# Performance work log

Hardware: AMD Instinct MI355X
Metric: run time of the kernel (lower is better)

## Reference

```python
import jax, jax.numpy as jnp
import numpy as np

B, T, C, H = 4, 2048, 1024, 16
D = C // H


def setup_inputs() -> dict:
    key = jax.random.key(0)
    ks = jax.random.split(key, 6)
    s = 1.0 / np.sqrt(C)
    return {
        "x": jax.random.normal(ks[0], (B, T, C), dtype=jnp.float32),
        "attention_mask": jnp.ones((B, 1, T), dtype=jnp.int32),
        "Wq": jax.random.normal(ks[1], (C, C), dtype=jnp.float32) * s,
        "bq": jnp.zeros((C,), dtype=jnp.float32),
        "Wk": jax.random.normal(ks[2], (C, C), dtype=jnp.float32) * s,
        "bk": jnp.zeros((C,), dtype=jnp.float32),
        "Wv": jax.random.normal(ks[3], (C, C), dtype=jnp.float32) * s,
        "bv": jnp.zeros((C,), dtype=jnp.float32),
        "Wp": jax.random.normal(ks[4], (C, C), dtype=jnp.float32) * s,
        "bp": jnp.zeros((C,), dtype=jnp.float32),
    }


def reference(x, attention_mask, Wq, bq, Wk, bk, Wv, bv, Wp, bp):
    b, t, c = x.shape
    d = c // H
    # projections (torch Linear: x @ W^T + b)
    q = (x @ Wq.T + bq).reshape(b, t, H, d).transpose(0, 2, 1, 3)  # [B,H,T,D]
    k = (x @ Wk.T + bk).reshape(b, t, H, d).transpose(0, 2, 1, 3)
    v = (x @ Wv.T + bv).reshape(b, t, H, d).transpose(0, 2, 1, 3)
    attn = jnp.einsum("bhqd,bhkd->bhqk", q, k) / jnp.sqrt(jnp.asarray(d, x.dtype))
    mask = attention_mask[:, :, :t]  # [B,1,T] -> broadcast over [B,H,T,T] keys
    attn = jnp.where(mask[:, :, None, :] == 0, jnp.asarray(-jnp.inf, x.dtype), attn)
    attn = jax.nn.softmax(attn, axis=-1)  # dropout p=0 (eval)
    y = jnp.einsum("bhqk,bhkd->bhqd", attn, v)
    y = y.transpose(0, 2, 1, 3).reshape(b, t, c)
    return y @ Wp.T + bp
```

## Files before the change

### kernel.cpp

```cpp
#include <hip/hip_runtime.h>


#define TT 2048
#define CC 1024
#define HH 16
#define DD 64
#define BB 4

typedef unsigned short u16;
typedef unsigned int u32;
typedef __attribute__((ext_vector_type(8))) short bf16x8;
typedef __attribute__((ext_vector_type(4))) float f32x4;

#if __has_builtin(__builtin_amdgcn_exp2f)
#define EXP2(x) __builtin_amdgcn_exp2f(x)
#else
#define EXP2(x) __expf((x) * 0.6931471805599453f)
#endif

__device__ __forceinline__ u16 f2bf(float f) {
    u32 u = __builtin_bit_cast(u32, f);
    u += 0x7FFFu + ((u >> 16) & 1u);
    return (u16)(u >> 16);
}
__device__ __forceinline__ u32 pk2(float a, float b) {
    u32 ua = __builtin_bit_cast(u32, a); ua += 0x7FFFu + ((ua >> 16) & 1u);
    u32 ub = __builtin_bit_cast(u32, b); ub += 0x7FFFu + ((ub >> 16) & 1u);
    return __builtin_amdgcn_perm(ub, ua, 0x07060302);
}

#define GLDS(g, l) __builtin_amdgcn_global_load_lds( \
    (const __attribute__((address_space(1))) void*)(g), \
    (__attribute__((address_space(3))) void*)(l), 16, 0, 0)

__global__ __launch_bounds__(256) void wcvt(const float* __restrict__ s,
                                            u16* __restrict__ d, int n8) {
    const int i = blockIdx.x * 256 + threadIdx.x;
    if (i < n8) {
        const float4 f0 = ((const float4*)s)[2 * i];
        const float4 f1 = ((const float4*)s)[2 * i + 1];
        uint4 w;
        w.x = pk2(f0.x, f0.y); w.y = pk2(f0.z, f0.w);
        w.z = pk2(f1.x, f1.y); w.w = pk2(f1.z, f1.w);
        ((uint4*)d)[i] = w;
    }
}

__global__ __launch_bounds__(256) void wcvt3(const float* __restrict__ s0,
                                             const float* __restrict__ s1,
                                             const float* __restrict__ s2,
                                             u16* __restrict__ d0,
                                             u16* __restrict__ d1,
                                             u16* __restrict__ d2, int n8) {
    const int which = blockIdx.y;
    const float* s = (which == 0) ? s0 : (which == 1) ? s1 : s2;
    u16* d = (which == 0) ? d0 : (which == 1) ? d1 : d2;
    const int i = blockIdx.x * 256 + threadIdx.x;
    if (i < n8) {
        const float4 f0 = ((const float4*)s)[2 * i];
        const float4 f1 = ((const float4*)s)[2 * i + 1];
        uint4 w;
        w.x = pk2(f0.x, f0.y); w.y = pk2(f0.z, f0.w);
        w.z = pk2(f1.x, f1.y); w.w = pk2(f1.z, f1.w);
        ((uint4*)d)[i] = w;
    }
}

template <int PROJ>
__global__ __launch_bounds__(256) void gemmX(const u16* __restrict__ A,
                                             const u16* __restrict__ Wb,
                                             const float* __restrict__ b0,
                                             const float* __restrict__ b1,
                                             const float* __restrict__ b2,
                                             void* __restrict__ out0,
                                             void* __restrict__ out1,
                                             void* __restrict__ out2) {
    __shared__ u16 As[128 * 64];
    __shared__ u16 Bs[128 * 64];

    const int tid  = threadIdx.x;
    const int wave = tid >> 6, lane = tid & 63;
    const int quad = lane >> 4, l16 = lane & 15;
    const int bm = blockIdx.y * 128, bn = blockIdx.x * 128;
    const int wm = (wave >> 1) * 64, wn = (wave & 1) * 64;
    const int K = CC;

    f32x4 acc[4][4] = {};

    for (int k0 = 0; k0 < K; k0 += 64) {
#pragma unroll
        for (int rr = 0; rr < 4; rr++) {
            const int c = rr * 256 + tid;
            const int row = c >> 3;
            const int cs = ((c & 7) ^ (row & 7)) * 8;
            GLDS(&Wb[(size_t)(bn + row) * K + k0 + cs], &Bs[c * 8]);
        }
#pragma unroll
        for (int rr = 0; rr < 4; rr++) {
            const int c = rr * 256 + tid;
            const int row = c >> 3;
            const int cs = ((c & 7) ^ (row & 7)) * 8;
            GLDS(&A[(size_t)(bm + row) * K + k0 + cs], &As[c * 8]);
        }
        __syncthreads();

#pragma unroll
        for (int ks = 0; ks < 2; ks++) {
            bf16x8 af[4], bfr[4];
#pragma unroll
            for (int i = 0; i < 4; i++) {
                const int row = wm + i * 16 + l16;
                const int s8 = (ks * 4 + quad) ^ (row & 7);
                af[i] = *(bf16x8*)&As[row * 64 + s8 * 8];
            }
#pragma unroll
            for (int j = 0; j < 4; j++) {
                const int row = wn + j * 16 + l16;
                const int s8 = (ks * 4 + quad) ^ (row & 7);
                bfr[j] = *(bf16x8*)&Bs[row * 64 + s8 * 8];
            }
#pragma unroll
            for (int i = 0; i < 4; i++)
#pragma unroll
                for (int j = 0; j < 4; j++)
                    acc[i][j] = __builtin_amdgcn_mfma_f32_16x16x32_bf16(af[i], bfr[j], acc[i][j], 0, 0, 0);
        }
        __syncthreads();
    }

    if (PROJ) {
        float* out = (float*)out0;
#pragma unroll
        for (int j = 0; j < 4; j++) {
            const int col = bn + wn + j * 16 + l16;
            const float bv = b0[col];
#pragma unroll
            for (int i = 0; i < 4; i++) {
                const int row0 = bm + wm + i * 16 + quad * 4;
#pragma unroll
                for (int r = 0; r < 4; r++)
                    out[(size_t)(row0 + r) * CC + col] = acc[i][j][r] + bv;
            }
        }
    } else {
        const int mid = bn >> 10;
        const float* bias = (mid == 0) ? b0 : (mid == 1) ? b1 : b2;
#pragma unroll
        for (int j = 0; j < 4; j++) {
            const int col  = bn + wn + j * 16 + l16;
            const int colL = col & (CC - 1);
            const float bv = bias[colL];
#pragma unroll
            for (int i = 0; i < 4; i++) {
                const int row0 = bm + wm + i * 16 + quad * 4;
                if (mid < 2) {
                    u16* out = (u16*)(mid ? out1 : out0);
#pragma unroll
                    for (int r = 0; r < 4; r++)
                        out[(size_t)(row0 + r) * CC + colL] = f2bf(acc[i][j][r] + bv);
                } else {
                    const int hh = colL >> 6, dch = colL & 63;
                    const int bb = row0 >> 11, t0 = row0 & (TT - 1);
                    const size_t idx = (((size_t)bb * HH + hh) * DD + dch) * TT + t0;
                    uint2 w;
                    w.x = pk2(acc[i][j][0] + bv, acc[i][j][1] + bv);
                    w.y = pk2(acc[i][j][2] + bv, acc[i][j][3] + bv);
                    *(uint2*)&((u16*)out2)[idx] = w;
                }
            }
        }
    }
}

__global__ __launch_bounds__(256) void attn(const u16* __restrict__ Q,
                                            const u16* __restrict__ Kb,
                                            const u16* __restrict__ Vt,
                                            const int* __restrict__ mask,
                                            u16* __restrict__ Y) {
    const int b = blockIdx.z, h = blockIdx.y, qt = blockIdx.x;
    const int tid  = threadIdx.x;
    const int wave = tid >> 6, lane = tid & 63;
    const int quad = lane >> 4, l16 = lane & 15;
    const int qrow0 = qt * 128 + wave * 32;

    __shared__ u16 Ks[2][64 * 64];
    __shared__ u16 Vs[2][64 * 64];
    __shared__ u16 Plds[4][32][72];

    const size_t qb = ((size_t)b * TT + qrow0) * CC + h * DD;

    bf16x8 qf[2][2];
#pragma unroll
    for (int m = 0; m < 2; m++)
#pragma unroll
        for (int ks = 0; ks < 2; ks++)
            qf[m][ks] = *(const bf16x8*)&Q[qb + (size_t)(m * 16 + l16) * CC + ks * 32 + quad * 8];

    const int c0 = tid, c1 = tid + 256;
    const int r0 = c0 >> 3, r1 = c1 >> 3;
    const int kp0 = (c0 & 7) ^ ((r0 >> 2) & 7), kp1 = (c1 & 7) ^ ((r1 >> 2) & 7);
    const int vp0 = (c0 & 7) ^ (r0 & 7),        vp1 = (c1 & 7) ^ (r1 & 7);
    const u16* kgp = Kb + ((size_t)b * TT) * CC + h * DD;
    const u16* vgp = Vt + ((size_t)(b * HH + h) * DD) * TT;
    const int* mp = mask + b * TT + 4 * l16;

    f32x4 o[2][4] = {};
    float lsum[2][4] = {};
    const float SC = 0.18033688011112042f;

    GLDS(&kgp[(size_t)r0 * CC + kp0 * 8], &Ks[0][c0 * 8]);
    GLDS(&kgp[(size_t)r1 * CC + kp1 * 8], &Ks[0][c1 * 8]);
    GLDS(&vgp[(size_t)r0 * TT + vp0 * 8], &Vs[0][c0 * 8]);
    GLDS(&vgp[(size_t)r1 * TT + vp1 * 8], &Vs[0][c1 * 8]);
    asm volatile("s_waitcnt vmcnt(0)" ::: "memory");
    __builtin_amdgcn_s_barrier();
    __builtin_amdgcn_sched_barrier(0);

#pragma unroll 1
    for (int kt = 0; kt < TT; kt += 64) {
        const int cur = (kt >> 6) & 1;
        const u16* Kc = &Ks[cur][0];
        const u16* Vc = &Vs[cur][0];

        const int4 mv = *(const int4*)&mp[kt];

        if (kt + 64 < TT) {
            const int nxt = cur ^ 1;
            GLDS(&kgp[(size_t)(kt + 64 + r0) * CC + kp0 * 8], &Ks[nxt][c0 * 8]);
            GLDS(&kgp[(size_t)(kt + 64 + r1) * CC + kp1 * 8], &Ks[nxt][c1 * 8]);
            GLDS(&vgp[(size_t)r0 * TT + kt + 64 + vp0 * 8], &Vs[nxt][c0 * 8]);
            GLDS(&vgp[(size_t)r1 * TT + kt + 64 + vp1 * 8], &Vs[nxt][c1 * 8]);
        }

        f32x4 s[2][4] = {};
        __builtin_amdgcn_s_setprio(1);
#pragma unroll
        for (int n = 0; n < 4; n++) {
#pragma unroll
            for (int ks = 0; ks < 2; ks++) {
                const int krow = 4 * l16 + n;
                const int pos = (ks * 4 + quad) ^ ((krow >> 2) & 7);
                const bf16x8 kf = *(bf16x8*)&Kc[krow * 64 + pos * 8];
#pragma unroll
                for (int m = 0; m < 2; m++)
                    s[m][n] = __builtin_amdgcn_mfma_f32_16x16x32_bf16(qf[m][ks], kf, s[m][n], 0, 0, 0);
            }
        }
        __builtin_amdgcn_s_setprio(0);

        float bb[4];
        bb[0] = mv.x ? 0.f : -1e38f;
        bb[1] = mv.y ? 0.f : -1e38f;
        bb[2] = mv.z ? 0.f : -1e38f;
        bb[3] = mv.w ? 0.f : -1e38f;

#pragma unroll
        for (int m = 0; m < 2; m++)
#pragma unroll
            for (int r = 0; r < 4; r++) {
                const float p0 = EXP2(fmaf(s[m][0][r], SC, bb[0]));
                const float p1 = EXP2(fmaf(s[m][1][r], SC, bb[1]));
                const float p2 = EXP2(fmaf(s[m][2][r], SC, bb[2]));
                const float p3 = EXP2(fmaf(s[m][3][r], SC, bb[3]));
                lsum[m][r] += (p0 + p1) + (p2 + p3);
                uint2 w; w.x = pk2(p0, p1); w.y = pk2(p2, p3);
                *(uint2*)&Plds[wave][m * 16 + quad * 4 + r][4 * l16] = w;
            }

        __builtin_amdgcn_s_setprio(1);
#pragma unroll
        for (int ks = 0; ks < 2; ks++) {
            bf16x8 pf[2];
#pragma unroll
            for (int m = 0; m < 2; m++)
                pf[m] = *(bf16x8*)&Plds[wave][m * 16 + l16][ks * 32 + quad * 8];
#pragma unroll
            for (int dt = 0; dt < 4; dt++) {
                const int vrow = dt * 16 + l16;
                const int pos = (ks * 4 + quad) ^ (vrow & 7);
                const bf16x8 vf = *(bf16x8*)&Vc[vrow * 64 + pos * 8];
#pragma unroll
                for (int m = 0; m < 2; m++)
                    o[m][dt] = __builtin_amdgcn_mfma_f32_16x16x32_bf16(pf[m], vf, o[m][dt], 0, 0, 0);
            }
        }
        __builtin_amdgcn_s_setprio(0);

        asm volatile("s_waitcnt vmcnt(0)" ::: "memory");
        __builtin_amdgcn_sched_barrier(0);
        __builtin_amdgcn_s_barrier();
    }

#pragma unroll
    for (int off = 1; off < 16; off <<= 1)
#pragma unroll
        for (int m = 0; m < 2; m++)
#pragma unroll
            for (int r = 0; r < 4; r++) lsum[m][r] += __shfl_xor(lsum[m][r], off, 64);

#pragma unroll
    for (int m = 0; m < 2; m++) {
        float inv[4];
#pragma unroll
        for (int r = 0; r < 4; r++) inv[r] = 1.0f / lsum[m][r];
#pragma unroll
        for (int dt = 0; dt < 4; dt++)
#pragma unroll
            for (int r = 0; r < 4; r++)
                Y[qb + (size_t)(m * 16 + quad * 4 + r) * CC + dt * 16 + l16] = f2bf(o[m][dt][r] * inv[r]);
    }
}

extern "C" void kernel_launch(void* const* d_in, const int* in_sizes, int n_in,
                              void* d_out, int out_size, void* d_ws, size_t ws_size,
                              hipStream_t stream) {
    const float* x    = (const float*)d_in[0];
    const int*   mask = (const int*)d_in[1];
    const float* Wq   = (const float*)d_in[2];
    const float* bq   = (const float*)d_in[3];
    const float* Wk   = (const float*)d_in[4];
    const float* bk   = (const float*)d_in[5];
    const float* Wv   = (const float*)d_in[6];
    const float* bv   = (const float*)d_in[7];
    const float* Wp   = (const float*)d_in[8];
    const float* bp   = (const float*)d_in[9];

    u16* ws = (u16*)d_ws;
    const size_t sz = (size_t)BB * TT * CC;
    u16* Qb   = ws;
    u16* Kbuf = ws + sz;
    u16* Vtb  = ws + 2 * sz;

    u16* xb   = (u16*)d_out;
    u16* Wq16 = xb + sz;
    u16* Wk16 = Wq16 + (size_t)CC * CC;
    u16* Wv16 = Wk16 + (size_t)CC * CC;

    const int W8 = CC * CC / 8;
    wcvt<<<4096, 256, 0, stream>>>(x, xb, (int)(sz / 8));
    wcvt3<<<dim3(512, 3), 256, 0, stream>>>(Wq, Wk, Wv, Wq16, Wk16, Wv16, W8);

    gemmX<0><<<dim3(24, 64), 256, 0, stream>>>(xb, Wq16, bq, bk, bv, Qb, Kbuf, Vtb);

    attn<<<dim3(TT / 128, HH, BB), 256, 0, stream>>>(Qb, Kbuf, Vtb, mask, Qb);

    wcvt<<<512, 256, 0, stream>>>(Wp, Kbuf, W8);
    gemmX<1><<<dim3(8, 64), 256, 0, stream>>>(Qb, Kbuf, bp, nullptr, nullptr, d_out, nullptr, nullptr);
}
```

Baseline: 310.3 us.

## Compute transposed QK^T scores to keep P in registers, skipping LDS round trip

```diff
diff --git a/kernel.cpp b/kernel.cpp
--- a/kernel.cpp
+++ b/kernel.cpp
@@ -11,6 +11,7 @@
 typedef unsigned int u32;
 typedef __attribute__((ext_vector_type(8))) short bf16x8;
 typedef __attribute__((ext_vector_type(4))) float f32x4;
+typedef __attribute__((ext_vector_type(4))) u32 u32x4;
 
 #if __has_builtin(__builtin_amdgcn_exp2f)
 #define EXP2(x) __builtin_amdgcn_exp2f(x)
@@ -27,6 +28,11 @@
     u32 ua = __builtin_bit_cast(u32, a); ua += 0x7FFFu + ((ua >> 16) & 1u);
     u32 ub = __builtin_bit_cast(u32, b); ub += 0x7FFFu + ((ub >> 16) & 1u);
     return __builtin_amdgcn_perm(ub, ua, 0x07060302);
+}
+__device__ __forceinline__ u32 cvtpk(float lo, float hi) {
+    u32 r;
+    asm("v_cvt_pk_bf16_f32 %0, %1, %2" : "=v"(r) : "v"(lo), "v"(hi));
+    return r;
 }
 
 #define GLDS(g, l) __builtin_amdgcn_global_load_lds( \
@@ -185,7 +191,7 @@
 
     __shared__ u16 Ks[2][64 * 64];
     __shared__ u16 Vs[2][64 * 64];
-    __shared__ u16 Plds[4][32][72];
+    __shared__ __align__(16) float bias_lds[TT];
 
     const size_t qb = ((size_t)b * TT + qrow0) * CC + h * DD;
 
@@ -196,23 +202,40 @@
         for (int ks = 0; ks < 2; ks++)
             qf[m][ks] = *(const bf16x8*)&Q[qb + (size_t)(m * 16 + l16) * CC + ks * 32 + quad * 8];
 
+    {
+        const int i = tid * 8;
+        const int4 m0 = *(const int4*)&mask[b * TT + i];
+        const int4 m1 = *(const int4*)&mask[b * TT + i + 4];
+        bias_lds[i + 0] = m0.x ? 0.f : -1e38f;
+        bias_lds[i + 1] = m0.y ? 0.f : -1e38f;
+        bias_lds[i + 2] = m0.z ? 0.f : -1e38f;
+        bias_lds[i + 3] = m0.w ? 0.f : -1e38f;
+        bias_lds[i + 4] = m1.x ? 0.f : -1e38f;
+        bias_lds[i + 5] = m1.y ? 0.f : -1e38f;
+        bias_lds[i + 6] = m1.z ? 0.f : -1e38f;
+        bias_lds[i + 7] = m1.w ? 0.f : -1e38f;
+    }
+
     const int c0 = tid, c1 = tid + 256;
     const int r0 = c0 >> 3, r1 = c1 >> 3;
-    const int kp0 = (c0 & 7) ^ ((r0 >> 2) & 7), kp1 = (c1 & 7) ^ ((r1 >> 2) & 7);
-    const int vp0 = (c0 & 7) ^ (r0 & 7),        vp1 = (c1 & 7) ^ (r1 & 7);
+    const int kp0 = (c0 & 7) ^ ((((r0 >> 3) & 1) << 2) | (r0 & 3));
+    const int kp1 = (c1 & 7) ^ ((((r1 >> 3) & 1) << 2) | (r1 & 3));
+    const int vp0 = (c0 & 7) ^ (r0 & 7), vp1 = (c1 & 7) ^ (r1 & 7);
     const u16* kgp = Kb + ((size_t)b * TT) * CC + h * DD;
     const u16* vgp = Vt + ((size_t)(b * HH + h) * DD) * TT;
-    const int* mp = mask + b * TT + 4 * l16;
+
+    const int rowA = ((l16 >> 2) << 3) | (l16 & 3);
+    const int s0k  = (((l16 >> 2) & 1) << 2) | (l16 & 3);
 
     f32x4 o[2][4] = {};
-    float lsum[2][4] = {};
+    float lsum[2] = {};
     const float SC = 0.18033688011112042f;
 
     GLDS(&kgp[(size_t)r0 * CC + kp0 * 8], &Ks[0][c0 * 8]);
     GLDS(&kgp[(size_t)r1 * CC + kp1 * 8], &Ks[0][c1 * 8]);
     GLDS(&vgp[(size_t)r0 * TT + vp0 * 8], &Vs[0][c0 * 8]);
     GLDS(&vgp[(size_t)r1 * TT + vp1 * 8], &Vs[0][c1 * 8]);
-    asm volatile("s_waitcnt vmcnt(0)" ::: "memory");
+    asm volatile("s_waitcnt vmcnt(0) lgkmcnt(0)" ::: "memory");
     __builtin_amdgcn_s_barrier();
     __builtin_amdgcn_sched_barrier(0);
 
@@ -221,8 +244,6 @@
         const int cur = (kt >> 6) & 1;
         const u16* Kc = &Ks[cur][0];
         const u16* Vc = &Vs[cur][0];
-
-        const int4 mv = *(const int4*)&mp[kt];
 
         if (kt + 64 < TT) {
             const int nxt = cur ^ 1;
@@ -232,53 +253,60 @@
             GLDS(&vgp[(size_t)r1 * TT + kt + 64 + vp1 * 8], &Vs[nxt][c1 * 8]);
         }
 
-        f32x4 s[2][4] = {};
+        const f32x4 bA = *(const f32x4*)&bias_lds[kt + quad * 8];
+        const f32x4 bB = *(const f32x4*)&bias_lds[kt + quad * 8 + 4];
+        const f32x4 bC = *(const f32x4*)&bias_lds[kt + 32 + quad * 8];
+        const f32x4 bD = *(const f32x4*)&bias_lds[kt + 32 + quad * 8 + 4];
+
+        f32x4 s2[2][4] = {};
         __builtin_amdgcn_s_setprio(1);
 #pragma unroll
         for (int n = 0; n < 4; n++) {
+            const int rowK = rowA + (n & 1) * 4 + (n >> 1) * 32;
 #pragma unroll
             for (int ks = 0; ks < 2; ks++) {
-                const int krow = 4 * l16 + n;
-                const int pos = (ks * 4 + quad) ^ ((krow >> 2) & 7);
-                const bf16x8 kf = *(bf16x8*)&Kc[krow * 64 + pos * 8];
+                const int pos = ((ks << 2) + quad) ^ s0k;
+                const bf16x8 kf = *(const bf16x8*)&Kc[rowK * 64 + pos * 8];
 #pragma unroll
                 for (int m = 0; m < 2; m++)
-                    s[m][n] = __builtin_amdgcn_mfma_f32_16x16x32_bf16(qf[m][ks], kf, s[m][n], 0, 0, 0);
+                    s2[m][n] = __builtin_amdgcn_mfma_f32_16x16x32_bf16(kf, qf[m][ks], s2[m][n], 0, 0, 0);
             }
         }
         __builtin_amdgcn_s_setprio(0);
 
-        float bb[4];
-        bb[0] = mv.x ? 0.f : -1e38f;
-        bb[1] = mv.y ? 0.f : -1e38f;
-        bb[2] = mv.z ? 0.f : -1e38f;
-        bb[3] = mv.w ? 0.f : -1e38f;
-
-#pragma unroll
-        for (int m = 0; m < 2; m++)
-#pragma unroll
-            for (int r = 0; r < 4; r++) {
-                const float p0 = EXP2(fmaf(s[m][0][r], SC, bb[0]));
-                const float p1 = EXP2(fmaf(s[m][1][r], SC, bb[1]));
-                const float p2 = EXP2(fmaf(s[m][2][r], SC, bb[2]));
-                const float p3 = EXP2(fmaf(s[m][3][r], SC, bb[3]));
-                lsum[m][r] += (p0 + p1) + (p2 + p3);
-                uint2 w; w.x = pk2(p0, p1); w.y = pk2(p2, p3);
-                *(uint2*)&Plds[wave][m * 16 + quad * 4 + r][4 * l16] = w;
-            }
+        u32 pkk[2][8];
+#pragma unroll
+        for (int m = 0; m < 2; m++) {
+            float ls = 0.f;
+#pragma unroll
+            for (int n = 0; n < 4; n++) {
+                const f32x4 bv = (n == 0) ? bA : (n == 1) ? bB : (n == 2) ? bC : bD;
+                const float p0 = EXP2(fmaf(s2[m][n][0], SC, bv[0]));
+                const float p1 = EXP2(fmaf(s2[m][n][1], SC, bv[1]));
+                const float p2 = EXP2(fmaf(s2[m][n][2], SC, bv[2]));
+                const float p3 = EXP2(fmaf(s2[m][n][3], SC, bv[3]));
+                ls += (p0 + p1) + (p2 + p3);
+                pkk[m][2 * n]     = cvtpk(p0, p1);
+                pkk[m][2 * n + 1] = cvtpk(p2, p3);
+            }
+            lsum[m] += ls;
+        }
 
         __builtin_amdgcn_s_setprio(1);
 #pragma unroll
         for (int ks = 0; ks < 2; ks++) {
             bf16x8 pf[2];
 #pragma unroll
-            for (int m = 0; m < 2; m++)
-                pf[m] = *(bf16x8*)&Plds[wave][m * 16 + l16][ks * 32 + quad * 8];
+            for (int m = 0; m < 2; m++) {
+                const u32x4 t = { pkk[m][4 * ks + 0], pkk[m][4 * ks + 1],
+                                  pkk[m][4 * ks + 2], pkk[m][4 * ks + 3] };
+                pf[m] = __builtin_bit_cast(bf16x8, t);
+            }
 #pragma unroll
             for (int dt = 0; dt < 4; dt++) {
                 const int vrow = dt * 16 + l16;
-                const int pos = (ks * 4 + quad) ^ (vrow & 7);
-                const bf16x8 vf = *(bf16x8*)&Vc[vrow * 64 + pos * 8];
+                const int pos = ((ks << 2) + quad) ^ (vrow & 7);
+                const bf16x8 vf = *(const bf16x8*)&Vc[vrow * 64 + pos * 8];
 #pragma unroll
                 for (int m = 0; m < 2; m++)
                     o[m][dt] = __builtin_amdgcn_mfma_f32_16x16x32_bf16(pf[m], vf, o[m][dt], 0, 0, 0);
@@ -292,17 +320,17 @@
     }
 
 #pragma unroll
-    for (int off = 1; off < 16; off <<= 1)
-#pragma unroll
-        for (int m = 0; m < 2; m++)
-#pragma unroll
-            for (int r = 0; r < 4; r++) lsum[m][r] += __shfl_xor(lsum[m][r], off, 64);
+    for (int m = 0; m < 2; m++) {
+        lsum[m] += __shfl_xor(lsum[m], 16, 64);
+        lsum[m] += __shfl_xor(lsum[m], 32, 64);
+    }
 
 #pragma unroll
     for (int m = 0; m < 2; m++) {
         float inv[4];
 #pragma unroll
-        for (int r = 0; r < 4; r++) inv[r] = 1.0f / lsum[m][r];
+        for (int r = 0; r < 4; r++)
+            inv[r] = 1.0f / __shfl(lsum[m], quad * 4 + r, 64);
 #pragma unroll
         for (int dt = 0; dt < 4; dt++)
 #pragma unroll
```

New measurement: 312.1 us. No clear change (+0.6%).
